# Optimization experiments

Measured on AMD Instinct MI355X. Metric: run time of the kernel, lower is better.

## Reference

```python
import jax, jax.numpy as jnp
import numpy as np

B, L, LC, C, CTX, H = 4, 2048, 512, 1024, 1024, 16
D = C // H
EPS = 1e-6
SCALE = 1.0 / np.float32(np.sqrt(D))


def _ln(x):
    # LayerNorm32, elementwise_affine applied outside when present
    mu = jnp.mean(x, axis=-1, keepdims=True)
    var = jnp.var(x, axis=-1, keepdims=True)
    return (x - mu) * jax.lax.rsqrt(var + EPS)


def _attn(q, k, v):
    # q: [B,Lq,H,D], k/v: [B,Lk,H,D] -> [B,Lq,C]
    s = jnp.einsum('bqhd,bkhd->bhqk', q, k) * SCALE
    p = jax.nn.softmax(s, axis=-1)
    o = jnp.einsum('bhqk,bkhd->bqhd', p, v)
    return o.reshape(o.shape[0], o.shape[1], C)


def setup_inputs() -> dict:
    key = jax.random.key(0)
    ks = jax.random.split(key, 12)
    s = 0.02
    w = lambda k, shape: (jax.random.normal(k, shape, jnp.float32) * s)
    z = lambda n: jnp.zeros((n,), jnp.float32)
    return {
        'x': jax.random.normal(ks[0], (B, L, C), jnp.float32),
        'mod': jax.random.normal(ks[1], (B, C), jnp.float32),
        'context': jax.random.normal(ks[2], (B, LC, CTX), jnp.float32),
        'w_ada': w(ks[3], (C, 6 * C)), 'b_ada': z(6 * C),
        'w_qkv': w(ks[4], (C, 3 * C)), 'b_qkv': z(3 * C),
        'w_so': w(ks[5], (C, C)), 'b_so': z(C),
        'g_n2': jnp.ones((C,), jnp.float32), 'b_n2': z(C),
        'w_cq': w(ks[6], (C, C)), 'b_cq': z(C),
        'w_ckv': w(ks[7], (CTX, 2 * C)), 'b_ckv': z(2 * C),
        'w_co': w(ks[8], (C, C)), 'b_co': z(C),
        'w_m1': w(ks[9], (C, 4 * C)), 'b_m1': z(4 * C),
        'w_m2': w(ks[10], (4 * C, C)), 'b_m2': z(C),
    }


def reference(x, mod, context, w_ada, b_ada, w_qkv, b_qkv, w_so, b_so,
              g_n2, b_n2, w_cq, b_cq, w_ckv, b_ckv, w_co, b_co,
              w_m1, b_m1, w_m2, b_m2):
    # adaLN modulation: SiLU -> Linear(C, 6C) -> chunk(6)
    ada = jax.nn.silu(mod) @ w_ada + b_ada  # [B, 6C]
    sh_msa, sc_msa, g_msa, sh_mlp, sc_mlp, g_mlp = jnp.split(ada, 6, axis=-1)
    ex = lambda t: t[:, None, :]  # broadcast per-sample over its token run

    # --- MSA branch ---
    h = _ln(x) * (1.0 + ex(sc_msa)) + ex(sh_msa)
    qkv = (h @ w_qkv + b_qkv).reshape(B, L, 3, H, D)
    h = _attn(qkv[:, :, 0], qkv[:, :, 1], qkv[:, :, 2]) @ w_so + b_so
    x = x + h * ex(g_msa)

    # --- MCA branch (norm2 has affine) ---
    h = _ln(x) * g_n2 + b_n2
    q = (h @ w_cq + b_cq).reshape(B, L, H, D)
    kv = (context @ w_ckv + b_ckv).reshape(B, LC, 2, H, D)
    h = _attn(q, kv[:, :, 0], kv[:, :, 1]) @ w_co + b_co
    x = x + h

    # --- FFN branch ---
    h = _ln(x) * (1.0 + ex(sc_mlp)) + ex(sh_mlp)
    h = jax.nn.gelu(h @ w_m1 + b_m1, approximate=False) @ w_m2 + b_m2
    x = x + h * ex(g_mlp)
    return x
```

## Files before the change

### kernel.cpp

```cpp
#include <hip/hip_runtime.h>
#include <cstdint>

typedef __bf16 bf16;
typedef __bf16 bf16x8 __attribute__((ext_vector_type(8)));
typedef __bf16 bf16x4 __attribute__((ext_vector_type(4)));
typedef float  floatx4 __attribute__((ext_vector_type(4)));
typedef unsigned int uint32x4 __attribute__((ext_vector_type(4)));

#define B_  4
#define L_  2048
#define LC_ 512
#define C_  1024
#define H_  16
#define D_  64

typedef const __attribute__((address_space(1))) unsigned int* as1_u32p;
typedef __attribute__((address_space(3))) unsigned int* as3_u32p;

__device__ __forceinline__ void async16(const void* g, void* l) {
  __builtin_amdgcn_global_load_lds((as1_u32p)g, (as3_u32p)l, 16, 0, 0);
}

__device__ __forceinline__ floatx4 mfma16(bf16x8 a, bf16x8 b, floatx4 c) {
  return __builtin_amdgcn_mfma_f32_16x16x32_bf16(a, b, c, 0, 0, 0);
}

__device__ __forceinline__ bool dt_bf16(const unsigned* dt) { return dt[0] == 0x3F803F80u; }

__device__ __forceinline__ float rd(const void* p, size_t i, bool bf) {
  return bf ? (float)((const bf16*)p)[i] : ((const float*)p)[i];
}

__global__ __launch_bounds__(256) void k_cvt(const void* __restrict__ src, bf16* __restrict__ dst,
                                             int N, const unsigned* __restrict__ dt) {
  bool bf = dt_bf16(dt);
  int i = (blockIdx.x * 256 + threadIdx.x) * 4;
  if (i + 3 < N) {
    for (int j = 0; j < 4; ++j) dst[i + j] = (bf16)rd(src, i + j, bf);
  } else {
    for (int j = 0; j < 4 && i + j < N; ++j) dst[i + j] = (bf16)rd(src, i + j, bf);
  }
}

struct CvtSrcs { const void* s[9]; };
__global__ __launch_bounds__(256) void k_cvt_all(CvtSrcs c, bf16* __restrict__ dst,
                                                 const unsigned* __restrict__ dt) {
  bool bf = dt_bf16(dt);
  int i = blockIdx.x * 256 + threadIdx.x;
  if (i >= 15360) return;
  const int pre[10] = {0, 3072, 4096, 5120, 6144, 7168, 9216, 10240, 14336, 15360};
  int seg = 0;
  #pragma unroll
  for (int k = 1; k < 9; ++k) if (i >= pre[k]) seg = k;
  dst[i] = (bf16)rd(c.s[seg], i - pre[seg], bf);
}

__global__ __launch_bounds__(256) void k_silu(const void* __restrict__ mod, float* __restrict__ sm,
                                              const unsigned* __restrict__ dt) {
  bool bf = dt_bf16(dt);
  int i = blockIdx.x * 256 + threadIdx.x;
  if (i < B_ * C_) {
    float v = rd(mod, i, bf);
    sm[i] = v / (1.f + __expf(-v));
  }
}

__global__ __launch_bounds__(256) void k_ada(const float* __restrict__ sm, const void* __restrict__ w,
                                             float* __restrict__ part, const unsigned* __restrict__ dt) {
  bool bf = dt_bf16(dt);
  int idx = blockIdx.x * 256 + threadIdx.x;
  int b = idx / 6144, j = idx - b * 6144;
  int k0 = blockIdx.y * 256;
  const float* s = sm + b * C_;
  float acc = 0.f;
  if (bf) {
    const bf16* W = (const bf16*)w;
    for (int k = k0; k < k0 + 256; ++k) acc += s[k] * (float)W[(size_t)k * 6144 + j];
  } else {
    const float* W = (const float*)w;
    for (int k = k0; k < k0 + 256; ++k) acc += s[k] * W[(size_t)k * 6144 + j];
  }
  part[(size_t)blockIdx.y * 24576 + idx] = acc;
}

__global__ __launch_bounds__(256) void k_ada_red(const float* __restrict__ part, const void* __restrict__ bv,
                                                 float* __restrict__ ada, const unsigned* __restrict__ dt) {
  bool bf = dt_bf16(dt);
  int idx = blockIdx.x * 256 + threadIdx.x;
  int j = idx % 6144;
  ada[idx] = rd(bv, j, bf) + part[idx] + part[24576 + idx] + part[49152 + idx] + part[73728 + idx];
}

struct TransDesc { const void* src; bf16* dst; int R, Cc, nCb, pre; };
struct TransDescs { TransDesc d[7]; };
__global__ __launch_bounds__(256) void k_trans_all(TransDescs t, const unsigned* __restrict__ dt) {
  bool bf = dt_bf16(dt);
  __shared__ bf16 tile[32][33];
  int blk = blockIdx.x;
  int di = 0;
  #pragma unroll
  for (int i = 1; i < 7; ++i) if (blk >= t.d[i].pre) di = i;
  const void* src = t.d[di].src;
  bf16* dst = t.d[di].dst;
  int R = t.d[di].R, Cc = t.d[di].Cc;
  int local = blk - t.d[di].pre;
  int bx = local % t.d[di].nCb, by = local / t.d[di].nCb;
  int c0 = bx * 32, r0 = by * 32;
  int tx = threadIdx.x & 31, ty = threadIdx.x >> 5;
  for (int i = 0; i < 4; ++i)
    tile[ty * 4 + i][tx] = (bf16)rd(src, (size_t)(r0 + ty * 4 + i) * Cc + c0 + tx, bf);
  __syncthreads();
  for (int i = 0; i < 4; ++i)
    dst[(size_t)(c0 + ty * 4 + i) * R + r0 + tx] = tile[tx][ty * 4 + i];
}

__global__ __launch_bounds__(256) void k_vt(const bf16* __restrict__ src, int ld, int off, int Lk,
                                            bf16* __restrict__ VT) {
  __shared__ bf16 tile[32][33];
  int l0 = blockIdx.x * 32;
  int d0 = blockIdx.y * 32;
  int bh = blockIdx.z, b = bh >> 4, h = bh & 15;
  int tx = threadIdx.x & 31, ty = threadIdx.x >> 5;
  for (int i = 0; i < 4; ++i) {
    int l = l0 + ty * 4 + i;
    tile[ty * 4 + i][tx] = src[((size_t)b * Lk + l) * ld + off + h * 64 + d0 + tx];
  }
  __syncthreads();
  for (int i = 0; i < 4; ++i) {
    int d = d0 + ty * 4 + i;
    VT[((size_t)bh * 64 + d) * Lk + l0 + tx] = tile[tx][ty * 4 + i];
  }
}

__global__ __launch_bounds__(256) void k_ln(const void* __restrict__ xraw, const float* __restrict__ xf,
                                            const unsigned* __restrict__ dt, bf16* __restrict__ out,
                                            const float* __restrict__ ada, int scOff, int shOff, float scAdd,
                                            const bf16* __restrict__ gcol, const bf16* __restrict__ bcol) {
  int row = blockIdx.x;
  int b = row >> 11;
  int base = row * C_ + threadIdx.x * 4;
  float v[4];
  if (xf) {
    for (int i = 0; i < 4; ++i) v[i] = xf[base + i];
  } else {
    bool bf = dt_bf16(dt);
    for (int i = 0; i < 4; ++i) v[i] = rd(xraw, base + i, bf);
  }
  float s1 = 0.f, s2 = 0.f;
  for (int i = 0; i < 4; ++i) { s1 += v[i]; s2 += v[i] * v[i]; }
  for (int m = 1; m < 64; m <<= 1) { s1 += __shfl_xor(s1, m); s2 += __shfl_xor(s2, m); }
  __shared__ float r1[4], r2[4];
  int w = threadIdx.x >> 6;
  if ((threadIdx.x & 63) == 0) { r1[w] = s1; r2[w] = s2; }
  __syncthreads();
  s1 = r1[0] + r1[1] + r1[2] + r1[3];
  s2 = r2[0] + r2[1] + r2[2] + r2[3];
  float mu = s1 * (1.f / (float)C_);
  float var = fmaxf(s2 * (1.f / (float)C_) - mu * mu, 0.f);
  float rstd = rsqrtf(var + 1e-6f);
  for (int i = 0; i < 4; ++i) {
    int c = threadIdx.x * 4 + i;
    float sc, sh;
    if (ada) { sc = scAdd + ada[b * 6144 + scOff + c]; sh = ada[b * 6144 + shOff + c]; }
    else     { sc = (float)gcol[c];                    sh = (float)bcol[c]; }
    out[base + i] = (bf16)((v[i] - mu) * rstd * sc + sh);
  }
}

template <int MODE>
__global__ __launch_bounds__(256) void k_gemm(const bf16* __restrict__ A, const bf16* __restrict__ Bt,
                                              const bf16* __restrict__ bias, void* __restrict__ outv,
                                              int M, int N, int K,
                                              const void* __restrict__ resid,
                                              const float* __restrict__ ada, int gateOff,
                                              const unsigned* __restrict__ dt,
                                              float qs, int qN) {
  __shared__ bf16 As[2 * 128 * 32];
  __shared__ bf16 Bs[2 * 128 * 32];
  const int tid = threadIdx.x;
  const int w = tid >> 6, lane = tid & 63;
  const int wr = w & 1, wc = w >> 1;
  const int g = lane >> 4, t = lane & 15;

  const int nbx = gridDim.x;
  const int nwg = nbx * gridDim.y;
  const int orig = blockIdx.y * nbx + blockIdx.x;
  const int qq = nwg >> 3, rrm = nwg & 7;
  const int xcd = orig & 7, sidx = orig >> 3;
  const int wgid = (xcd < rrm ? xcd * (qq + 1) : rrm * (qq + 1) + (xcd - rrm) * qq) + sidx;
  const int rowA0 = (wgid / nbx) * 128, rowB0 = (wgid % nbx) * 128;

  const bf16* Ag = A  + (size_t)(rowA0 + w * 32 + (lane >> 2)) * K + (lane & 3) * 8;
  const bf16* Bg = Bt + (size_t)(rowB0 + w * 32 + (lane >> 2)) * K + (lane & 3) * 8;
  bf16* As0 = As + w * 1024;
  bf16* Bs0 = Bs + w * 1024;

  floatx4 acc[4][4];
  for (int i = 0; i < 4; ++i) for (int j = 0; j < 4; ++j) for (int r = 0; r < 4; ++r) acc[i][j][r] = 0.f;

  for (int kb = 0; kb < K; kb += 64) {
    async16(Ag + kb,                      As0);
    async16(Ag + kb + (size_t)16 * K,     As0 + 512);
    async16(Ag + kb + 32,                 As0 + 4096);
    async16(Ag + kb + 32 + (size_t)16 * K, As0 + 4096 + 512);
    async16(Bg + kb,                      Bs0);
    async16(Bg + kb + (size_t)16 * K,     Bs0 + 512);
    async16(Bg + kb + 32,                 Bs0 + 4096);
    async16(Bg + kb + 32 + (size_t)16 * K, Bs0 + 4096 + 512);
    __syncthreads();
    #pragma unroll
    for (int kk = 0; kk < 2; ++kk) {
      bf16x8 af[4], bfr[4];
      #pragma unroll
      for (int mt = 0; mt < 4; ++mt) af[mt]  = *(const bf16x8*)&As[kk * 4096 + (wr * 64 + mt * 16 + t) * 32 + g * 8];
      #pragma unroll
      for (int nt = 0; nt < 4; ++nt) bfr[nt] = *(const bf16x8*)&Bs[kk * 4096 + (wc * 64 + nt * 16 + t) * 32 + g * 8];
      #pragma unroll
      for (int mt = 0; mt < 4; ++mt)
        #pragma unroll
        for (int nt = 0; nt < 4; ++nt)
          acc[mt][nt] = mfma16(af[mt], bfr[nt], acc[mt][nt]);
    }
    __syncthreads();
  }

  const bool bf = (MODE == 1 || MODE == 4) ? dt_bf16(dt) : false;
  for (int mt = 0; mt < 4; ++mt) {
    for (int nt = 0; nt < 4; ++nt) {
      int grow = rowA0 + wr * 64 + mt * 16 + g * 4;
      int gcol = rowB0 + wc * 64 + nt * 16 + t;
      float bvv = (float)bias[gcol];
      for (int r = 0; r < 4; ++r) {
        int rr = grow + r;
        float v = acc[mt][nt][r] + bvv;
        size_t idx = (size_t)rr * N + gcol;
        if (MODE == 0) {
          ((bf16*)outv)[idx] = (bf16)(v * ((gcol < qN) ? qs : 1.0f));
        } else if (MODE == 1) {
          float gt = ada[(rr >> 11) * 6144 + gateOff + gcol];
          ((float*)outv)[idx] = rd(resid, idx, bf) + v * gt;
        } else if (MODE == 2) {
          ((float*)outv)[idx] = ((const float*)resid)[idx] + v;
        } else if (MODE == 3) {
          ((bf16*)outv)[idx] = (bf16)(0.5f * v * (1.f + erff(v * 0.70710678118654752f)));
        } else {
          float gt = ada[(rr >> 11) * 6144 + gateOff + gcol];
          float val = ((const float*)resid)[idx] + v * gt;
          if (bf) ((bf16*)outv)[idx] = (bf16)val;
          else    ((float*)outv)[idx] = val;
        }
      }
    }
  }
}

__global__ __launch_bounds__(256) void k_attn(const bf16* __restrict__ Qb, int ldq, int qoff,
                                              const bf16* __restrict__ Kb, int ldk, int koff,
                                              const bf16* __restrict__ VT,
                                              bf16* __restrict__ Ob, int Lk) {
  __shared__ bf16 smem[20480];

  const int tid = threadIdx.x;
  const int w = tid >> 6, lane = tid & 63;
  const int g = lane >> 4, t = lane & 15;
  const int bh = blockIdx.y, b = bh >> 4, h = bh & 15;
  const int q0 = blockIdx.x * 64;

  const bf16* Q  = Qb + (size_t)(b * L_ + q0) * ldq + h * 64 + qoff;
  const bf16* K  = Kb + (size_t)b * Lk * ldk + h * 64 + koff;
  const bf16* Vt = VT + (size_t)bh * 64 * Lk;
  bf16* O = Ob + ((size_t)(b * L_ + q0 + w * 16 + t)) * C_ + h * 64;

  const int sr0 = w * 16 + (lane >> 3), sp = lane & 7;
  const int sr1 = sr0 + 8;
  const int sw0 = (sp ^ (sr0 & 7)) * 8;
  const int sw1 = (sp ^ (sr1 & 7)) * 8;

  bf16* Ps  = smem;
  bf16* Kb0 = smem + 4096;
  bf16* Vb0 = smem + 12288;

  async16(Q + (size_t)sr0 * ldq + sw0, smem + w * 1024);
  async16(Q + (size_t)sr1 * ldq + sw1, smem + w * 1024 + 512);
  async16(K + (size_t)sr0 * ldk + sw0, Kb0 + w * 1024);
  async16(K + (size_t)sr1 * ldk + sw1, Kb0 + w * 1024 + 512);
  async16(Vt + (size_t)sr0 * Lk + sw0, Vb0 + w * 1024);
  async16(Vt + (size_t)sr1 * Lk + sw1, Vb0 + w * 1024 + 512);
  __syncthreads();

  const int rowQ = w * 16 + t;
  bf16x8 bq[2];
  #pragma unroll
  for (int ko = 0; ko < 2; ++ko)
    bq[ko] = *(const bf16x8*)&smem[rowQ * 64 + (((ko * 4 + g) ^ (rowQ & 7)) * 8)];

  float l_run = 0.f;
  floatx4 o_acc[4];
  for (int d = 0; d < 4; ++d) for (int r = 0; r < 4; ++r) o_acc[d][r] = 0.f;

  int cur = 0;
  for (int kt = 0; kt < Lk; kt += 64) {
    const bf16* Kc = Kb0 + cur * 4096;
    const bf16* Vc = Vb0 + cur * 4096;

    if (kt + 64 < Lk) {
      int nx = kt + 64;
      bf16* Kn = Kb0 + (cur ^ 1) * 4096 + w * 1024;
      bf16* Vn = Vb0 + (cur ^ 1) * 4096 + w * 1024;
      async16(K + (size_t)(nx + sr0) * ldk + sw0, Kn);
      async16(K + (size_t)(nx + sr1) * ldk + sw1, Kn + 512);
      async16(Vt + (size_t)sr0 * Lk + nx + sw0, Vn);
      async16(Vt + (size_t)sr1 * Lk + nx + sw1, Vn + 512);
    }

    floatx4 s[4];
    __builtin_amdgcn_s_setprio(1);
    #pragma unroll
    for (int mt = 0; mt < 4; ++mt) {
      floatx4 sa; for (int r = 0; r < 4; ++r) sa[r] = 0.f;
      #pragma unroll
      for (int ko = 0; ko < 2; ++ko) {
        int rowK = mt * 16 + t;
        bf16x8 ak = *(const bf16x8*)&Kc[rowK * 64 + (((ko * 4 + g) ^ (rowK & 7)) * 8)];
        sa = mfma16(ak, bq[ko], sa);
      }
      s[mt] = sa;
    }
    __builtin_amdgcn_s_setprio(0);

    float sv[16];
    float sum = 0.f;
    #pragma unroll
    for (int mt = 0; mt < 4; ++mt)
      #pragma unroll
      for (int r = 0; r < 4; ++r) { float e = exp2f(s[mt][r]); sv[mt * 4 + r] = e; sum += e; }
    sum += __shfl_xor(sum, 16);
    sum += __shfl_xor(sum, 32);
    l_run += sum;

    #pragma unroll
    for (int mt = 0; mt < 4; ++mt) {
      bf16x4 pk;
      for (int r = 0; r < 4; ++r) pk[r] = (bf16)sv[mt * 4 + r];
      int off = mt * 16 + g * 4;
      int chunk = off >> 3, sub = off & 7;
      *(bf16x4*)&Ps[rowQ * 64 + ((chunk ^ (rowQ & 7)) * 8) + sub] = pk;
    }

    __builtin_amdgcn_s_setprio(1);
    #pragma unroll
    for (int ko = 0; ko < 2; ++ko) {
      bf16x8 bp = *(const bf16x8*)&Ps[rowQ * 64 + (((ko * 4 + g) ^ (rowQ & 7)) * 8)];
      #pragma unroll
      for (int d = 0; d < 4; ++d) {
        int rowV = d * 16 + t;
        bf16x8 av = *(const bf16x8*)&Vc[rowV * 64 + (((ko * 4 + g) ^ (rowV & 7)) * 8)];
        o_acc[d] = mfma16(av, bp, o_acc[d]);
      }
    }
    __builtin_amdgcn_s_setprio(0);

    cur ^= 1;
    __syncthreads();
  }

  float rl = 1.f / l_run;
  #pragma unroll
  for (int d = 0; d < 4; ++d) {
    bf16x4 ov;
    for (int r = 0; r < 4; ++r) ov[r] = (bf16)(o_acc[d][r] * rl);
    *(bf16x4*)&O[d * 16 + g * 4] = ov;
  }
}

extern "C" void kernel_launch(void* const* d_in, const int* in_sizes, int n_in,
                              void* d_out, int out_size, void* d_ws, size_t ws_size,
                              hipStream_t stream) {
  const void* x     = d_in[0];
  const void* mod   = d_in[1];
  const void* ctx   = d_in[2];
  const void* w_ada = d_in[3];
  const void* b_ada = d_in[4];
  const void* w_qkv = d_in[5];
  const void* b_qkv = d_in[6];
  const void* w_so  = d_in[7];
  const void* b_so  = d_in[8];
  const void* g_n2  = d_in[9];
  const void* b_n2  = d_in[10];
  const void* w_cq  = d_in[11];
  const void* b_cq  = d_in[12];
  const void* w_ckv = d_in[13];
  const void* b_ckv = d_in[14];
  const void* w_co  = d_in[15];
  const void* b_co  = d_in[16];
  const void* w_m1  = d_in[17];
  const void* b_m1  = d_in[18];
  const void* w_m2  = d_in[19];
  const void* b_m2  = d_in[20];
  const unsigned* dt = (const unsigned*)g_n2;

  char* p = (char*)d_ws;
  auto alloc = [&](size_t bytes) { char* r = p; p += (bytes + 255) & ~(size_t)255; return r; };
  float* sm    = (float*)alloc((size_t)B_ * C_ * 4);
  float* adp   = (float*)alloc((size_t)4 * 24576 * 4);
  float* ada   = (float*)alloc((size_t)B_ * 6144 * 4);
  bf16* wT_qkv = (bf16*)alloc((size_t)3072 * 1024 * 2);
  bf16* wT_so  = (bf16*)alloc((size_t)1024 * 1024 * 2);
  bf16* wT_cq  = (bf16*)alloc((size_t)1024 * 1024 * 2);
  bf16* wT_ckv = (bf16*)alloc((size_t)2048 * 1024 * 2);
  bf16* wT_co  = (bf16*)alloc((size_t)1024 * 1024 * 2);
  bf16* wT_m1  = (bf16*)alloc((size_t)4096 * 1024 * 2);
  bf16* wT_m2  = (bf16*)alloc((size_t)1024 * 4096 * 2);
  bf16* hb     = (bf16*)alloc((size_t)8192 * 1024 * 2);
  bf16* qkvb   = (bf16*)alloc((size_t)8192 * 3072 * 2);
  bf16* attn_o = (bf16*)alloc((size_t)8192 * 1024 * 2);
  float* xcur  = (float*)alloc((size_t)8192 * 1024 * 4);
  bf16* ctxb   = (bf16*)alloc((size_t)B_ * LC_ * 1024 * 2);
  bf16* biasb  = (bf16*)alloc(15360 * 2);
  bf16* bqkvb = biasb;
  bf16* bsob  = biasb + 3072;
  bf16* g2b   = biasb + 4096;
  bf16* b2b   = biasb + 5120;
  bf16* bcqb  = biasb + 6144;
  bf16* bckvb = biasb + 7168;
  bf16* bcob  = biasb + 9216;
  bf16* bm1b  = biasb + 10240;
  bf16* bm2b  = biasb + 14336;
  bf16* q2   = qkvb;
  bf16* kv   = qkvb + (size_t)8192 * 1024;
  bf16* gbuf = qkvb;
  bf16* vt   = hb;
  if (ws_size < (size_t)(p - (char*)d_ws)) return;

  dim3 blk(256);
  k_silu<<<16, blk, 0, stream>>>(mod, sm, dt);
  k_ada<<<dim3(96, 4), blk, 0, stream>>>(sm, w_ada, adp, dt);
  k_ada_red<<<96, blk, 0, stream>>>(adp, b_ada, ada, dt);
  k_cvt<<<2048, blk, 0, stream>>>(ctx, ctxb, B_ * LC_ * 1024, dt);
  CvtSrcs cs = {{b_qkv, b_so, g_n2, b_n2, b_cq, b_ckv, b_co, b_m1, b_m2}};
  k_cvt_all<<<60, blk, 0, stream>>>(cs, biasb, dt);
  TransDescs td = {{
    {w_qkv, wT_qkv, 1024, 3072,  96, 0},
    {w_so,  wT_so,  1024, 1024,  32, 3072},
    {w_cq,  wT_cq,  1024, 1024,  32, 4096},
    {w_ckv, wT_ckv, 1024, 2048,  64, 5120},
    {w_co,  wT_co,  1024, 1024,  32, 7168},
    {w_m1,  wT_m1,  1024, 4096, 128, 8192},
    {w_m2,  wT_m2,  4096, 1024,  32, 12288},
  }};
  k_trans_all<<<16384, blk, 0, stream>>>(td, dt);

  const float SC_L2E = 0.125f * 1.44269504088896f;

  k_ln<<<8192, blk, 0, stream>>>(x, nullptr, dt, hb, ada, 1024, 0, 1.0f, nullptr, nullptr);
  k_gemm<0><<<dim3(24, 64), blk, 0, stream>>>(hb, wT_qkv, bqkvb, qkvb, 8192, 3072, 1024, nullptr, nullptr, 0, dt, SC_L2E, 1024);
  k_vt<<<dim3(64, 2, 64), blk, 0, stream>>>(qkvb, 3072, 2048, L_, vt);
  k_attn<<<dim3(32, 64), blk, 0, stream>>>(qkvb, 3072, 0, qkvb, 3072, 1024, vt, attn_o, L_);
  k_gemm<1><<<dim3(8, 64), blk, 0, stream>>>(attn_o, wT_so, bsob, xcur, 8192, 1024, 1024, x, ada, 2048, dt, 1.f, 0);

  k_ln<<<8192, blk, 0, stream>>>(nullptr, xcur, dt, hb, nullptr, 0, 0, 0.f, g2b, b2b);
  k_gemm<0><<<dim3(8, 64), blk, 0, stream>>>(hb, wT_cq, bcqb, q2, 8192, 1024, 1024, nullptr, nullptr, 0, dt, SC_L2E, 1024);
  k_gemm<0><<<dim3(16, 16), blk, 0, stream>>>(ctxb, wT_ckv, bckvb, kv, 2048, 2048, 1024, nullptr, nullptr, 0, dt, 1.f, 0);
  k_vt<<<dim3(16, 2, 64), blk, 0, stream>>>(kv, 2048, 1024, LC_, vt);
  k_attn<<<dim3(32, 64), blk, 0, stream>>>(q2, 1024, 0, kv, 2048, 0, vt, attn_o, LC_);
  k_gemm<2><<<dim3(8, 64), blk, 0, stream>>>(attn_o, wT_co, bcob, xcur, 8192, 1024, 1024, xcur, nullptr, 0, dt, 1.f, 0);

  k_ln<<<8192, blk, 0, stream>>>(nullptr, xcur, dt, hb, ada, 4096, 3072, 1.0f, nullptr, nullptr);
  k_gemm<3><<<dim3(32, 64), blk, 0, stream>>>(hb, wT_m1, bm1b, gbuf, 8192, 4096, 1024, nullptr, nullptr, 0, dt, 1.f, 0);
  k_gemm<4><<<dim3(8, 64), blk, 0, stream>>>(gbuf, wT_m2, bm2b, d_out, 8192, 1024, 4096, xcur, ada, 5120, dt, 1.f, 0);
}
```

Measured before the change: 877.9 us.

## Software-pipeline QK^T one tile ahead and compute row sums via MFMA

Restructures the attention inner loop so the QK^T MFMAs for the next key tile are issued between the exp/P-store of the current tile and the PV MFMAs, with K prefetched two tiles ahead and V one tile ahead. The softmax denominator is no longer summed with shuffles; it comes from an extra MFMA against a vector of ones on the bf16 P values. This is meant to overlap exp work with matrix work and drop the cross-lane reductions. In exchange it keeps more registers live and uses the bf16-rounded P for the sum, which changes numerics slightly.

```diff
diff --git a/kernel.cpp b/kernel.cpp
--- a/kernel.cpp
+++ b/kernel.cpp
@@ -277,15 +277,15 @@
   const int sw1 = (sp ^ (sr1 & 7)) * 8;
 
   bf16* Ps  = smem;
-  bf16* Kb0 = smem + 4096;
-  bf16* Vb0 = smem + 12288;
+  bf16* KB0 = smem + 4096;
+  bf16* VB0 = smem + 12288;
 
   async16(Q + (size_t)sr0 * ldq + sw0, smem + w * 1024);
   async16(Q + (size_t)sr1 * ldq + sw1, smem + w * 1024 + 512);
-  async16(K + (size_t)sr0 * ldk + sw0, Kb0 + w * 1024);
-  async16(K + (size_t)sr1 * ldk + sw1, Kb0 + w * 1024 + 512);
-  async16(Vt + (size_t)sr0 * Lk + sw0, Vb0 + w * 1024);
-  async16(Vt + (size_t)sr1 * Lk + sw1, Vb0 + w * 1024 + 512);
+  async16(K + (size_t)sr0 * ldk + sw0, KB0 + w * 1024);
+  async16(K + (size_t)sr1 * ldk + sw1, KB0 + w * 1024 + 512);
+  async16(Vt + (size_t)sr0 * Lk + sw0, VB0 + w * 1024);
+  async16(Vt + (size_t)sr1 * Lk + sw1, VB0 + w * 1024 + 512);
   __syncthreads();
 
   const int rowQ = w * 16 + t;
@@ -294,49 +294,58 @@
   for (int ko = 0; ko < 2; ++ko)
     bq[ko] = *(const bf16x8*)&smem[rowQ * 64 + (((ko * 4 + g) ^ (rowQ & 7)) * 8)];
 
-  float l_run = 0.f;
-  floatx4 o_acc[4];
+  const int nt = Lk >> 6;
+
+  if (nt > 1) {
+    async16(K + (size_t)(64 + sr0) * ldk + sw0, KB0 + 4096 + w * 1024);
+    async16(K + (size_t)(64 + sr1) * ldk + sw1, KB0 + 4096 + w * 1024 + 512);
+  }
+
+  floatx4 s[4];
+  __builtin_amdgcn_s_setprio(1);
+  #pragma unroll
+  for (int mt = 0; mt < 4; ++mt) {
+    floatx4 sa; for (int r = 0; r < 4; ++r) sa[r] = 0.f;
+    #pragma unroll
+    for (int ko = 0; ko < 2; ++ko) {
+      int rowK = mt * 16 + t;
+      bf16x8 ak = *(const bf16x8*)&KB0[rowK * 64 + (((ko * 4 + g) ^ (rowK & 7)) * 8)];
+      sa = mfma16(ak, bq[ko], sa);
+    }
+    s[mt] = sa;
+  }
+  __builtin_amdgcn_s_setprio(0);
+  __syncthreads();
+
+  bf16x8 ones;
+  #pragma unroll
+  for (int i = 0; i < 8; ++i) ones[i] = (bf16)1.0f;
+
+  floatx4 o_acc[4], o_sum;
   for (int d = 0; d < 4; ++d) for (int r = 0; r < 4; ++r) o_acc[d][r] = 0.f;
-
-  int cur = 0;
-  for (int kt = 0; kt < Lk; kt += 64) {
-    const bf16* Kc = Kb0 + cur * 4096;
-    const bf16* Vc = Vb0 + cur * 4096;
-
-    if (kt + 64 < Lk) {
-      int nx = kt + 64;
-      bf16* Kn = Kb0 + (cur ^ 1) * 4096 + w * 1024;
-      bf16* Vn = Vb0 + (cur ^ 1) * 4096 + w * 1024;
+  for (int r = 0; r < 4; ++r) o_sum[r] = 0.f;
+
+  for (int ti = 0; ti < nt; ++ti) {
+    const int cur = ti & 1;
+
+    if (ti + 2 < nt) {
+      int nx = (ti + 2) << 6;
+      bf16* Kn = KB0 + cur * 4096 + w * 1024;
       async16(K + (size_t)(nx + sr0) * ldk + sw0, Kn);
       async16(K + (size_t)(nx + sr1) * ldk + sw1, Kn + 512);
+    }
+    if (ti + 1 < nt) {
+      int nx = (ti + 1) << 6;
+      bf16* Vn = VB0 + ((ti + 1) & 1) * 4096 + w * 1024;
       async16(Vt + (size_t)sr0 * Lk + nx + sw0, Vn);
       async16(Vt + (size_t)sr1 * Lk + nx + sw1, Vn + 512);
     }
 
-    floatx4 s[4];
-    __builtin_amdgcn_s_setprio(1);
-    #pragma unroll
-    for (int mt = 0; mt < 4; ++mt) {
-      floatx4 sa; for (int r = 0; r < 4; ++r) sa[r] = 0.f;
-      #pragma unroll
-      for (int ko = 0; ko < 2; ++ko) {
-        int rowK = mt * 16 + t;
-        bf16x8 ak = *(const bf16x8*)&Kc[rowK * 64 + (((ko * 4 + g) ^ (rowK & 7)) * 8)];
-        sa = mfma16(ak, bq[ko], sa);
-      }
-      s[mt] = sa;
-    }
-    __builtin_amdgcn_s_setprio(0);
-
     float sv[16];
-    float sum = 0.f;
     #pragma unroll
     for (int mt = 0; mt < 4; ++mt)
       #pragma unroll
-      for (int r = 0; r < 4; ++r) { float e = exp2f(s[mt][r]); sv[mt * 4 + r] = e; sum += e; }
-    sum += __shfl_xor(sum, 16);
-    sum += __shfl_xor(sum, 32);
-    l_run += sum;
+      for (int r = 0; r < 4; ++r) sv[mt * 4 + r] = exp2f(s[mt][r]);
 
     #pragma unroll
     for (int mt = 0; mt < 4; ++mt) {
@@ -347,10 +356,29 @@
       *(bf16x4*)&Ps[rowQ * 64 + ((chunk ^ (rowQ & 7)) * 8) + sub] = pk;
     }
 
+    if (ti + 1 < nt) {
+      const bf16* Kc = KB0 + ((ti + 1) & 1) * 4096;
+      __builtin_amdgcn_s_setprio(1);
+      #pragma unroll
+      for (int mt = 0; mt < 4; ++mt) {
+        floatx4 sa; for (int r = 0; r < 4; ++r) sa[r] = 0.f;
+        #pragma unroll
+        for (int ko = 0; ko < 2; ++ko) {
+          int rowK = mt * 16 + t;
+          bf16x8 ak = *(const bf16x8*)&Kc[rowK * 64 + (((ko * 4 + g) ^ (rowK & 7)) * 8)];
+          sa = mfma16(ak, bq[ko], sa);
+        }
+        s[mt] = sa;
+      }
+      __builtin_amdgcn_s_setprio(0);
+    }
+
+    const bf16* Vc = VB0 + cur * 4096;
     __builtin_amdgcn_s_setprio(1);
     #pragma unroll
     for (int ko = 0; ko < 2; ++ko) {
       bf16x8 bp = *(const bf16x8*)&Ps[rowQ * 64 + (((ko * 4 + g) ^ (rowQ & 7)) * 8)];
+      o_sum = mfma16(ones, bp, o_sum);
       #pragma unroll
       for (int d = 0; d < 4; ++d) {
         int rowV = d * 16 + t;
@@ -360,11 +388,10 @@
     }
     __builtin_amdgcn_s_setprio(0);
 
-    cur ^= 1;
-    __syncthreads();
-  }
-
-  float rl = 1.f / l_run;
+    if (ti + 1 < nt) __syncthreads();
+  }
+
+  float rl = 1.f / o_sum[0];
   #pragma unroll
   for (int d = 0; d < 4; ++d) {
     bf16x4 ov;
```

Result: faster. 835.6 us (-4.8%).
